# Performance work log

Measured on AMD Instinct MI355X. Metric: run time of the kernel, lower is better.

## Reference

```python
import jax, jax.numpy as jnp
import numpy as np

B, C, H, W = 8, 256, 80, 160   # 1/8-resolution feature maps of a 640x1280 stereo pair
DISP = 192 // 8                 # cost volume depth at 1/8 res
FACTOR = 2 ** 3                 # convex-upsample factor (n_downsample=3)
TOP_K = 3


def setup_inputs() -> dict:
    key = jax.random.key(0)
    k1, k2, k3 = jax.random.split(key, 3)
    return {
        "left": jax.random.normal(k1, (B, C, H, W), dtype=jnp.float32),
        "right": jax.random.normal(k2, (B, C, H, W), dtype=jnp.float32),
        "mask": jax.random.normal(k3, (B, 9 * FACTOR * FACTOR, H, W), dtype=jnp.float32),
        "iters": 12,
    }


def build_cost_volume(left, right):
    # cost[b,i,h,w] = mean_c left[b,c,h,w] * right[b,c,h,w-i], zero where w < i
    slices = []
    for i in range(DISP):  # fixed small structural loop over disparity shifts
        prod = jnp.mean(left[:, :, :, i:] * right[:, :, :, : W - i if i > 0 else W], axis=1)
        prod = jnp.pad(prod, ((0, 0), (0, 0), (i, 0)))
        slices.append(prod)
    return jnp.stack(slices, axis=1)  # [B, DISP, H, W]


def regression_topk(cost, k=TOP_K):
    # top-k over the disparity axis, softmax-weighted expectation of indices
    c = jnp.moveaxis(cost, 1, -1)            # [B, H, W, DISP]
    vals, inds = jax.lax.top_k(c, k)          # descending, like torch sort(1, True)[:, :k]
    w = jax.nn.softmax(vals, axis=-1)
    disp = jnp.sum(w * inds.astype(vals.dtype), axis=-1)
    return disp[:, None]                      # [B, 1, H, W]


def convex_upsample(flow, mask, iters):
    # Upsample [H,W] flow -> [8H,8W] via softmax convex combination of 3x3 neighbors.
    N, D, Hh, Ww = flow.shape
    temp = 1.0 + jnp.exp(-(jnp.float32(iters) - 1.0))  # training-mode temperature
    m = mask.reshape(N, 1, 9, FACTOR, FACTOR, Hh, Ww)
    m = jax.nn.softmax(m / temp, axis=2)
    fp = jnp.pad(FACTOR * flow, ((0, 0), (0, 0), (1, 1), (1, 1)))
    # 3x3 unfold in torch F.unfold row-major order: (dy, dx)
    patches = jnp.stack(
        [fp[:, :, dy:dy + Hh, dx:dx + Ww] for dy in range(3) for dx in range(3)], axis=2
    )  # [N, D, 9, H, W]
    up = jnp.sum(m * patches[:, :, :, None, None], axis=2)   # [N, D, F, F, H, W]
    up = up.transpose(0, 1, 4, 2, 5, 3)                      # [N, D, H, F, W, F]
    return up.reshape(N, D, FACTOR * Hh, FACTOR * Ww)


def reference(left, right, mask, iters):
    cost = build_cost_volume(left, right)
    init_disp = regression_topk(cost)                               # [B,1,H,W]
    # flow field (x-disparity channel + frozen y channel, as delta_flow[:,1]=0)
    flow = jnp.concatenate([init_disp, jnp.zeros_like(init_disp)], axis=1)
    flow_up = convex_upsample(flow, mask, iters)                    # [B,2,8H,8W]
    return -flow_up[:, :1]                                          # disparity prediction
```

## Files before the change

kernel.cpp:

```cpp
#include <hip/hip_runtime.h>
#include <cmath>

#define NBATCH 8
#define NCH    256
#define NH     80
#define NW     160
#define NDISP  24
#define FAC    8

constexpr int CG   = 8;
constexpr int CPG  = NCH / CG;
constexpr int WQ   = NW / 4;
constexpr int TPB  = WQ * CG;
constexpr int ROWF = 348;
constexpr int BUFF = CG * ROWF;

__device__ __forceinline__ float f4c(const float4& v, int k) {
  switch (k) { case 0: return v.x; case 1: return v.y; case 2: return v.z; default: return v.w; }
}

__global__ __launch_bounds__(TPB) void cost_topk_kernel(
    const float* __restrict__ left, const float* __restrict__ right,
    float* __restrict__ disp)
{
  __shared__ float smem[2 * BUFF];

  const int t  = threadIdx.x;
  const int cg = t & 7;
  const int wq = t >> 3;
  const int w0 = wq * 4;
  const int b  = blockIdx.x / NH;
  const int h  = blockIdx.x % NH;

  const size_t hw = (size_t)NH * NW;
  const float* lrow = left  + (size_t)b * NCH * hw + (size_t)h * NW;
  const float* rrow = right + (size_t)b * NCH * hw + (size_t)h * NW;

  for (int q = t; q < 2 * CG * 6; q += TPB) {
    int buf = q / 48, ch = (q / 6) % 8, k = q % 6;
    *reinterpret_cast<float4*>(&smem[buf * BUFF + ch * ROWF + 160 + 4 * k]) = float4{0.f, 0.f, 0.f, 0.f};
  }

  const int qa = t, qb = t + TPB;
  const int chA = qa / 80, remA = qa % 80;
  const int chB = qb / 80, remB = qb % 80;
  const int ldsA = chA * ROWF + ((remA < 40) ? remA * 4 : 184 + (remA - 40) * 4);
  const int ldsB = chB * ROWF + ((remB < 40) ? remB * 4 : 184 + (remB - 40) * 4);
  const float* gA = ((remA < 40) ? lrow : rrow) + (size_t)chA * CPG * hw + ((remA < 40) ? remA * 4 : (remA - 40) * 4);
  const float* gB = ((remB < 40) ? lrow : rrow) + (size_t)chB * CPG * hw + ((remB < 40) ? remB * 4 : (remB - 40) * 4);

  float4 s0 = *reinterpret_cast<const float4*>(gA);
  float4 s1 = *reinterpret_cast<const float4*>(gB);

  float acc[NDISP][4];
#pragma unroll
  for (int i = 0; i < NDISP; ++i)
#pragma unroll
    for (int ws = 0; ws < 4; ++ws) acc[i][ws] = 0.f;

  for (int j = 0; j < CPG; ++j) {
    float* base = &smem[(j & 1) * BUFF];
    __syncthreads();
    *reinterpret_cast<float4*>(&base[ldsA]) = s0;
    *reinterpret_cast<float4*>(&base[ldsB]) = s1;
    if (j + 1 < CPG) {
      s0 = *reinterpret_cast<const float4*>(gA + (size_t)(j + 1) * hw);
      s1 = *reinterpret_cast<const float4*>(gB + (size_t)(j + 1) * hw);
    }
    __syncthreads();

    const float* row = base + cg * ROWF;
    float4 L  = *reinterpret_cast<const float4*>(row + w0);
    float4 Qa = *reinterpret_cast<const float4*>(row + 160 + w0);
#pragma unroll
    for (int g = 0; g < 6; ++g) {
      const int i0 = 20 - 4 * g;
      float4 Qb = *reinterpret_cast<const float4*>(row + 184 + w0 - i0);
#pragma unroll
      for (int di = 0; di < 4; ++di)
#pragma unroll
        for (int ws = 0; ws < 4; ++ws) {
          const int pos = ws - di + 4;
          float rv = (pos < 4) ? f4c(Qa, pos) : f4c(Qb, pos - 4);
          acc[i0 + di][ws] = __builtin_fmaf(f4c(L, ws), rv, acc[i0 + di][ws]);
        }
      Qa = Qb;
    }
  }

#pragma unroll
  for (int mskm = 1; mskm < 8; mskm <<= 1)
#pragma unroll
    for (int i = 0; i < NDISP; ++i)
#pragma unroll
      for (int ws = 0; ws < 4; ++ws)
        acc[i][ws] += __shfl_xor(acc[i][ws], mskm, 64);

  if (cg == 0) {
    float o[4];
#pragma unroll
    for (int ws = 0; ws < 4; ++ws) {
      float v1 = -1e30f, v2 = -1e30f, v3 = -1e30f;
      int   j1 = 0, j2 = 0, j3 = 0;
#pragma unroll
      for (int i = 0; i < NDISP; ++i) {
        float v = acc[i][ws] * 0.00390625f;
        if (v > v1)      { v3 = v2; j3 = j2; v2 = v1; j2 = j1; v1 = v; j1 = i; }
        else if (v > v2) { v3 = v2; j3 = j2; v2 = v;  j2 = i; }
        else if (v > v3) { v3 = v;  j3 = i; }
      }
      float e2 = expf(v2 - v1), e3 = expf(v3 - v1);
      float ssum = 1.0f + e2 + e3;
      o[ws] = ((float)j1 + e2 * (float)j2 + e3 * (float)j3) / ssum;
    }
    *reinterpret_cast<float4*>(&disp[((size_t)b * NH + h) * NW + w0]) = float4{o[0], o[1], o[2], o[3]};
  }
}

__global__ __launch_bounds__(256) void upsample_kernel(
    const float* __restrict__ disp, const float* __restrict__ mask,
    const int* __restrict__ itp, float* __restrict__ out)
{
  int idx = blockIdx.x * 256 + threadIdx.x;
  const int w  = idx % NW;
  const int fy = (idx / NW) & 7;
  const int h  = (idx / (NW * FAC)) % NH;
  const int b  = idx / (NW * FAC * NH);

  const float iters = (float)itp[0];
  const float temp  = 1.0f + __expf(-(iters - 1.0f));
  const float sc    = 1.44269504088896340736f / temp;

  const size_t hw = (size_t)NH * NW;
  const float* drow = disp + (size_t)b * hw;
  float d[9];
#pragma unroll
  for (int dy = 0; dy < 3; ++dy)
#pragma unroll
    for (int dx = 0; dx < 3; ++dx) {
      int h2 = h + dy - 1, w2 = w + dx - 1;
      bool ok = (h2 >= 0) && (h2 < NH) && (w2 >= 0) && (w2 < NW);
      d[dy * 3 + dx] = ok ? drow[h2 * NW + w2] : 0.f;
    }

  const float* mb = mask + (size_t)b * 576 * hw + (size_t)h * NW + w;
  float m[9][FAC];
#pragma unroll
  for (int j = 0; j < 9; ++j)
#pragma unroll
    for (int fx = 0; fx < FAC; ++fx)
      m[j][fx] = mb[(size_t)((j * 8 + fy) * 8 + fx) * hw];

  float o[FAC];
#pragma unroll
  for (int fx = 0; fx < FAC; ++fx) {
    float mx = m[0][fx];
#pragma unroll
    for (int j = 1; j < 9; ++j) mx = fmaxf(mx, m[j][fx]);
    float ssum = 0.f, accv = 0.f;
#pragma unroll
    for (int j = 0; j < 9; ++j) {
      float e = exp2f((m[j][fx] - mx) * sc);
      ssum += e;
      accv += e * d[j];
    }
    o[fx] = -8.0f * accv / ssum;
  }

  float* op = out + ((size_t)b * (NH * FAC) + (size_t)(h * FAC + fy)) * (NW * FAC) + (size_t)w * FAC;
  *reinterpret_cast<float4*>(op)     = float4{o[0], o[1], o[2], o[3]};
  *reinterpret_cast<float4*>(op + 4) = float4{o[4], o[5], o[6], o[7]};
}

extern "C" void kernel_launch(void* const* d_in, const int* in_sizes, int n_in,
                              void* d_out, int out_size, void* d_ws, size_t ws_size,
                              hipStream_t stream) {
  (void)in_sizes; (void)n_in; (void)out_size; (void)ws_size;
  const float* left  = (const float*)d_in[0];
  const float* right = (const float*)d_in[1];
  const float* mask  = (const float*)d_in[2];
  const int*   iters = (const int*)d_in[3];
  float* out  = (float*)d_out;
  float* disp = (float*)d_ws;

  hipLaunchKernelGGL(cost_topk_kernel, dim3(NBATCH * NH), dim3(TPB), 0, stream,
                     left, right, disp);
  hipLaunchKernelGGL(upsample_kernel, dim3(NBATCH * NH * FAC * NW / 256), dim3(256), 0, stream,
                     disp, mask, iters, out);
}
```

Measured before the change: 152.5 us.

## Replace LDS staging in cost kernel with direct register loads, double-buffered

The cost-volume kernel no longer stages left/right rows through shared memory with barriers. Each thread now loads its own left float4 and a 28-float window of right directly from global memory into registers, double-buffered across channel pairs, and the grid is flattened to 256-thread blocks. This removes LDS traffic and __syncthreads, at the cost of redundant global loads of overlapping right windows (relying on cache) and higher register pressure. The upsample division is also replaced by a hardware reciprocal multiply, which is slightly less precise.

New measurement: 192.8 us. +26.5%, slower.

```diff
diff --git a/kernel.cpp b/kernel.cpp
--- a/kernel.cpp
+++ b/kernel.cpp
@@ -8,49 +8,29 @@
 #define NDISP  24
 #define FAC    8
 
-constexpr int CG   = 8;
-constexpr int CPG  = NCH / CG;
-constexpr int WQ   = NW / 4;
-constexpr int TPB  = WQ * CG;
-constexpr int ROWF = 348;
-constexpr int BUFF = CG * ROWF;
+constexpr int CG  = 8;
+constexpr int CPG = NCH / CG;
 
 __device__ __forceinline__ float f4c(const float4& v, int k) {
   switch (k) { case 0: return v.x; case 1: return v.y; case 2: return v.z; default: return v.w; }
 }
 
-__global__ __launch_bounds__(TPB) void cost_topk_kernel(
+__global__ __launch_bounds__(256) void cost_topk_kernel(
     const float* __restrict__ left, const float* __restrict__ right,
     float* __restrict__ disp)
 {
-  __shared__ float smem[2 * BUFF];
-
-  const int t  = threadIdx.x;
-  const int cg = t & 7;
-  const int wq = t >> 3;
-  const int w0 = wq * 4;
-  const int b  = blockIdx.x / NH;
-  const int h  = blockIdx.x % NH;
+  const int gt  = blockIdx.x * 256 + threadIdx.x;
+  const int cg  = gt & 7;
+  const int wqf = gt >> 3;
+  const int wq  = wqf % 40;
+  const int row = wqf / 40;
+  const int b   = row / NH;
+  const int h   = row % NH;
+  const int w0  = wq * 4;
 
   const size_t hw = (size_t)NH * NW;
-  const float* lrow = left  + (size_t)b * NCH * hw + (size_t)h * NW;
-  const float* rrow = right + (size_t)b * NCH * hw + (size_t)h * NW;
-
-  for (int q = t; q < 2 * CG * 6; q += TPB) {
-    int buf = q / 48, ch = (q / 6) % 8, k = q % 6;
-    *reinterpret_cast<float4*>(&smem[buf * BUFF + ch * ROWF + 160 + 4 * k]) = float4{0.f, 0.f, 0.f, 0.f};
-  }
-
-  const int qa = t, qb = t + TPB;
-  const int chA = qa / 80, remA = qa % 80;
-  const int chB = qb / 80, remB = qb % 80;
-  const int ldsA = chA * ROWF + ((remA < 40) ? remA * 4 : 184 + (remA - 40) * 4);
-  const int ldsB = chB * ROWF + ((remB < 40) ? remB * 4 : 184 + (remB - 40) * 4);
-  const float* gA = ((remA < 40) ? lrow : rrow) + (size_t)chA * CPG * hw + ((remA < 40) ? remA * 4 : (remA - 40) * 4);
-  const float* gB = ((remB < 40) ? lrow : rrow) + (size_t)chB * CPG * hw + ((remB < 40) ? remB * 4 : (remB - 40) * 4);
-
-  float4 s0 = *reinterpret_cast<const float4*>(gA);
-  float4 s1 = *reinterpret_cast<const float4*>(gB);
+  const float* lp = left  + ((size_t)b * NCH + (size_t)cg * CPG) * hw + (size_t)h * NW + w0;
+  const float* rp = right + ((size_t)b * NCH + (size_t)cg * CPG) * hw + (size_t)h * NW + (w0 - 24);
 
   float acc[NDISP][4];
 #pragma unroll
@@ -58,34 +38,43 @@
 #pragma unroll
     for (int ws = 0; ws < 4; ++ws) acc[i][ws] = 0.f;
 
-  for (int j = 0; j < CPG; ++j) {
-    float* base = &smem[(j & 1) * BUFF];
-    __syncthreads();
-    *reinterpret_cast<float4*>(&base[ldsA]) = s0;
-    *reinterpret_cast<float4*>(&base[ldsB]) = s1;
-    if (j + 1 < CPG) {
-      s0 = *reinterpret_cast<const float4*>(gA + (size_t)(j + 1) * hw);
-      s1 = *reinterpret_cast<const float4*>(gB + (size_t)(j + 1) * hw);
+  auto loadset = [&](float4* rq, float4& lq, const float* l, const float* r) {
+    lq = *reinterpret_cast<const float4*>(l);
+    if (w0 >= 24) {
+#pragma unroll
+      for (int g = 0; g < 7; ++g)
+        rq[g] = *reinterpret_cast<const float4*>(r + 4 * g);
+    } else {
+#pragma unroll
+      for (int g = 0; g < 7; ++g) {
+        rq[g] = float4{0.f, 0.f, 0.f, 0.f};
+        if (w0 - 24 + 4 * g >= 0)
+          rq[g] = *reinterpret_cast<const float4*>(r + 4 * g);
+      }
     }
-    __syncthreads();
+  };
 
-    const float* row = base + cg * ROWF;
-    float4 L  = *reinterpret_cast<const float4*>(row + w0);
-    float4 Qa = *reinterpret_cast<const float4*>(row + 160 + w0);
+  auto fmaset = [&](const float4* rq, const float4& lq) {
 #pragma unroll
-    for (int g = 0; g < 6; ++g) {
-      const int i0 = 20 - 4 * g;
-      float4 Qb = *reinterpret_cast<const float4*>(row + 184 + w0 - i0);
+    for (int i = 0; i < NDISP; ++i)
 #pragma unroll
-      for (int di = 0; di < 4; ++di)
-#pragma unroll
-        for (int ws = 0; ws < 4; ++ws) {
-          const int pos = ws - di + 4;
-          float rv = (pos < 4) ? f4c(Qa, pos) : f4c(Qb, pos - 4);
-          acc[i0 + di][ws] = __builtin_fmaf(f4c(L, ws), rv, acc[i0 + di][ws]);
-        }
-      Qa = Qb;
-    }
+      for (int ws = 0; ws < 4; ++ws) {
+        const int e = 24 + ws - i;
+        acc[i][ws] = __builtin_fmaf(f4c(lq, ws), f4c(rq[e >> 2], e & 3), acc[i][ws]);
+      }
+  };
+
+  float4 LA, LB, A[7], B[7];
+  loadset(A, LA, lp, rp);
+  loadset(B, LB, lp + hw, rp + hw);
+  lp += 2 * hw; rp += 2 * hw;
+
+#pragma unroll 1
+  for (int jj = 0; jj < CPG; jj += 2) {
+    fmaset(A, LA);
+    if (jj + 2 < CPG) { loadset(A, LA, lp, rp); lp += hw; rp += hw; }
+    fmaset(B, LB);
+    if (jj + 3 < CPG) { loadset(B, LB, lp, rp); lp += hw; rp += hw; }
   }
 
 #pragma unroll
@@ -164,7 +153,7 @@
       ssum += e;
       accv += e * d[j];
     }
-    o[fx] = -8.0f * accv / ssum;
+    o[fx] = (-8.0f * accv) * __builtin_amdgcn_rcpf(ssum);
   }
 
   float* op = out + ((size_t)b * (NH * FAC) + (size_t)(h * FAC + fy)) * (NW * FAC) + (size_t)w * FAC;
@@ -183,7 +172,7 @@
   float* out  = (float*)d_out;
   float* disp = (float*)d_ws;
 
-  hipLaunchKernelGGL(cost_topk_kernel, dim3(NBATCH * NH), dim3(TPB), 0, stream,
+  hipLaunchKernelGGL(cost_topk_kernel, dim3(NBATCH * NH * 40 * CG / 256), dim3(256), 0, stream,
                      left, right, disp);
   hipLaunchKernelGGL(upsample_kernel, dim3(NBATCH * NH * FAC * NW / 256), dim3(256), 0, stream,
                      disp, mask, iters, out);
```

## Restructure cost-volume kernel into per-wave tiles with async global-to-LDS triple buffering

Applied to the files above, without the earlier changes.

The cost/top-k kernel moves from one block per row with block-wide double buffering and __syncthreads to independent wavefronts, each handling a 32-column tile. Each wave streams its left and right channel slices straight into XOR-swizzled LDS with global_load_lds, uses a three-deep buffer, and paces itself with vmcnt waits instead of barriers. The aim is to hide global load latency, raise occupancy, and cut LDS bank conflicts. The upsample division becomes a hardware reciprocal, which slightly lowers precision. The hand-written waitcnt scheduling is fragile, and the first tile relies on zero-filling the out-of-range halo.

New measurement: 134.4 us. -11.9%, faster.

```diff
diff --git a/kernel.cpp b/kernel.cpp
--- a/kernel.cpp
+++ b/kernel.cpp
@@ -8,49 +8,73 @@
 #define NDISP  24
 #define FAC    8
 
-constexpr int CG   = 8;
-constexpr int CPG  = NCH / CG;
-constexpr int WQ   = NW / 4;
-constexpr int TPB  = WQ * CG;
-constexpr int ROWF = 348;
-constexpr int BUFF = CG * ROWF;
+constexpr int TPB1  = 256;
+constexpr int WPB   = 4;
+constexpr int NTILE = 5;
+constexpr int SLOTS = 192;
+
+typedef __attribute__((address_space(1))) unsigned int gu32;
+typedef __attribute__((address_space(3))) unsigned int lu32;
+
+__device__ __forceinline__ void gload_lds16(const float* g, float4* l) {
+  __builtin_amdgcn_global_load_lds((gu32*)g, (lu32*)l, 16, 0, 0);
+}
+
+template <int N>
+__device__ __forceinline__ void wait_vm() {
+  if constexpr (N == 6)      asm volatile("s_waitcnt vmcnt(6)" ::: "memory");
+  else if constexpr (N == 3) asm volatile("s_waitcnt vmcnt(3)" ::: "memory");
+  else                       asm volatile("s_waitcnt vmcnt(0)" ::: "memory");
+  __builtin_amdgcn_sched_barrier(0);
+}
 
 __device__ __forceinline__ float f4c(const float4& v, int k) {
   switch (k) { case 0: return v.x; case 1: return v.y; case 2: return v.z; default: return v.w; }
 }
 
-__global__ __launch_bounds__(TPB) void cost_topk_kernel(
+__global__ __launch_bounds__(TPB1) void cost_topk_kernel(
     const float* __restrict__ left, const float* __restrict__ right,
     float* __restrict__ disp)
 {
-  __shared__ float smem[2 * BUFF];
-
-  const int t  = threadIdx.x;
-  const int cg = t & 7;
-  const int wq = t >> 3;
-  const int w0 = wq * 4;
-  const int b  = blockIdx.x / NH;
-  const int h  = blockIdx.x % NH;
+  __shared__ float4 lds4[WPB][3][SLOTS];
+
+  const int lane = threadIdx.x & 63;
+  const int widx = threadIdx.x >> 6;
+  const int wid  = blockIdx.x * WPB + widx;
+  const int tile = wid % NTILE;
+  const int row  = wid / NTILE;
+  const int b    = row / NH;
+  const int h    = row % NH;
+  const int wb   = tile * 32;
+
+  const int cg = lane & 7;
+  const int wq = lane >> 3;
 
   const size_t hw = (size_t)NH * NW;
   const float* lrow = left  + (size_t)b * NCH * hw + (size_t)h * NW;
   const float* rrow = right + (size_t)b * NCH * hw + (size_t)h * NW;
 
-  for (int q = t; q < 2 * CG * 6; q += TPB) {
-    int buf = q / 48, ch = (q / 6) % 8, k = q % 6;
-    *reinterpret_cast<float4*>(&smem[buf * BUFF + ch * ROWF + 160 + 4 * k]) = float4{0.f, 0.f, 0.f, 0.f};
-  }
-
-  const int qa = t, qb = t + TPB;
-  const int chA = qa / 80, remA = qa % 80;
-  const int chB = qb / 80, remB = qb % 80;
-  const int ldsA = chA * ROWF + ((remA < 40) ? remA * 4 : 184 + (remA - 40) * 4);
-  const int ldsB = chB * ROWF + ((remB < 40) ? remB * 4 : 184 + (remB - 40) * 4);
-  const float* gA = ((remA < 40) ? lrow : rrow) + (size_t)chA * CPG * hw + ((remA < 40) ? remA * 4 : (remA - 40) * 4);
-  const float* gB = ((remB < 40) ? lrow : rrow) + (size_t)chB * CPG * hw + ((remB < 40) ? remB * 4 : (remB - 40) * 4);
-
-  float4 s0 = *reinterpret_cast<const float4*>(gA);
-  float4 s1 = *reinterpret_cast<const float4*>(gB);
+  const int c0 = lane >> 4,        q0 = (lane & 15) ^ c0;
+  const int c1 = 4 + (lane >> 4),  q1 = (lane & 15) ^ c1;
+  const int cl = lane >> 3,        wqs = (lane & 7) ^ cl;
+
+  int off0 = wb - 32 + 4 * q0; if (off0 < 0) off0 = 0;
+  int off1 = wb - 32 + 4 * q1; if (off1 < 0) off1 = 0;
+
+  const float* srcR0 = rrow + (size_t)(c0 * 32) * hw + off0;
+  const float* srcR1 = rrow + (size_t)(c1 * 32) * hw + off1;
+  const float* srcL  = lrow + (size_t)(cl * 32) * hw + wb + 4 * wqs;
+
+#define STAGE(BUF) do {                              \
+    gload_lds16(srcR0, &lds4[widx][BUF][0]);         \
+    gload_lds16(srcR1, &lds4[widx][BUF][64]);        \
+    gload_lds16(srcL,  &lds4[widx][BUF][128]);       \
+    srcR0 += hw; srcR1 += hw; srcL += hw; } while (0)
+
+  int rsl[7];
+#pragma unroll
+  for (int k = 0; k < 7; ++k) rsl[k] = cg * 16 + ((wq + 2 + k) ^ cg);
+  const int lslot = 128 + cg * 8 + (wq ^ cg);
 
   float acc[NDISP][4];
 #pragma unroll
@@ -58,35 +82,49 @@
 #pragma unroll
     for (int ws = 0; ws < 4; ++ws) acc[i][ws] = 0.f;
 
-  for (int j = 0; j < CPG; ++j) {
-    float* base = &smem[(j & 1) * BUFF];
-    __syncthreads();
-    *reinterpret_cast<float4*>(&base[ldsA]) = s0;
-    *reinterpret_cast<float4*>(&base[ldsB]) = s1;
-    if (j + 1 < CPG) {
-      s0 = *reinterpret_cast<const float4*>(gA + (size_t)(j + 1) * hw);
-      s1 = *reinterpret_cast<const float4*>(gB + (size_t)(j + 1) * hw);
-    }
-    __syncthreads();
-
-    const float* row = base + cg * ROWF;
-    float4 L  = *reinterpret_cast<const float4*>(row + w0);
-    float4 Qa = *reinterpret_cast<const float4*>(row + 160 + w0);
+  auto fmastep = [&](const float4* base) {
+    float4 Lq = base[lslot];
+    float4 Qa = base[rsl[0]];
 #pragma unroll
     for (int g = 0; g < 6; ++g) {
+      float4 Qb = base[rsl[g + 1]];
       const int i0 = 20 - 4 * g;
-      float4 Qb = *reinterpret_cast<const float4*>(row + 184 + w0 - i0);
 #pragma unroll
       for (int di = 0; di < 4; ++di)
 #pragma unroll
         for (int ws = 0; ws < 4; ++ws) {
           const int pos = ws - di + 4;
           float rv = (pos < 4) ? f4c(Qa, pos) : f4c(Qb, pos - 4);
-          acc[i0 + di][ws] = __builtin_fmaf(f4c(L, ws), rv, acc[i0 + di][ws]);
+          acc[i0 + di][ws] = __builtin_fmaf(f4c(Lq, ws), rv, acc[i0 + di][ws]);
         }
       Qa = Qb;
     }
+  };
+
+  const float4 fzero{0.f, 0.f, 0.f, 0.f};
+
+#define STEP(VM, BUF, DOSTAGE) do {                                        \
+    wait_vm<VM>();                                                         \
+    if (tile == 0)         \
+      lds4[widx][BUF][(lane >> 3) * 16 + (lane & 7)] = fzero;              \
+    fmastep(&lds4[widx][BUF][0]);                                          \
+    if (DOSTAGE) {                                                         \
+      asm volatile("s_waitcnt lgkmcnt(0)" ::: "memory");                   \
+      __builtin_amdgcn_sched_barrier(0);                                   \
+      STAGE(BUF);                                                          \
+    } } while (0)
+
+  STAGE(0); STAGE(1); STAGE(2);
+
+  for (int it = 0; it < 10; ++it) {
+    STEP(6, 0, true);
+    STEP(6, 1, true);
+    STEP(6, 2, (it < 9));
   }
+  STEP(3, 0, false);
+  STEP(0, 1, false);
+#undef STEP
+#undef STAGE
 
 #pragma unroll
   for (int mskm = 1; mskm < 8; mskm <<= 1)
@@ -113,7 +151,8 @@
       float ssum = 1.0f + e2 + e3;
       o[ws] = ((float)j1 + e2 * (float)j2 + e3 * (float)j3) / ssum;
     }
-    *reinterpret_cast<float4*>(&disp[((size_t)b * NH + h) * NW + w0]) = float4{o[0], o[1], o[2], o[3]};
+    *reinterpret_cast<float4*>(&disp[((size_t)b * NH + h) * NW + wb + wq * 4]) =
+        float4{o[0], o[1], o[2], o[3]};
   }
 }
 
@@ -164,7 +203,7 @@
       ssum += e;
       accv += e * d[j];
     }
-    o[fx] = -8.0f * accv / ssum;
+    o[fx] = (-8.0f * accv) * __builtin_amdgcn_rcpf(ssum);
   }
 
   float* op = out + ((size_t)b * (NH * FAC) + (size_t)(h * FAC + fy)) * (NW * FAC) + (size_t)w * FAC;
@@ -183,7 +222,7 @@
   float* out  = (float*)d_out;
   float* disp = (float*)d_ws;
 
-  hipLaunchKernelGGL(cost_topk_kernel, dim3(NBATCH * NH), dim3(TPB), 0, stream,
+  hipLaunchKernelGGL(cost_topk_kernel, dim3(NBATCH * NH * NTILE / WPB), dim3(TPB1), 0, stream,
                      left, right, disp);
   hipLaunchKernelGGL(upsample_kernel, dim3(NBATCH * NH * FAC * NW / 256), dim3(256), 0, stream,
                      disp, mask, iters, out);
```
